# Optimization experiments

Measured on AMD Instinct MI355X. Metric: run time of the kernel, lower is better.

Reference implementation:

```python
import jax, jax.numpy as jnp
import numpy as np

B, T, D, DIM = 32, 2048, 1024, 1024


def setup_inputs() -> dict:
    key = jax.random.key(0)
    ks = jax.random.split(key, 7)
    def glorot(k, shape):
        lim = np.sqrt(6.0 / (shape[0] + shape[1]))
        return jax.random.uniform(k, shape, jnp.float32, -lim, lim)
    return {
        "input_states": jax.random.normal(ks[0], (B, T, D), jnp.float32),
        "last_state": jax.random.normal(ks[1], (B, D), jnp.float32),
        "Wy": glorot(ks[2], (D, DIM)),
        "Wh": glorot(ks[3], (D, DIM)),
        "w": glorot(ks[4], (DIM, 1)),
        "Wp": glorot(ks[5], (D, DIM)),
        "Wx": glorot(ks[6], (D, DIM)),
    }


def reference(input_states, last_state, Wy, Wh, w, Wp, Wx):
    # hs: (B,T,dim); last_state projection broadcast over T (the original
    # tiles last_state via a ones-matmul; a plain broadcast is the same math)
    hs = jnp.einsum("btd,de->bte", input_states, Wy)
    hproj = last_state @ Wh                      # (B,dim)
    m = jax.nn.relu(hs + hproj[:, None, :])      # (B,T,dim)
    scores = jnp.einsum("bte,eo->bt", m, w[:, :1])  # squeeze last dim
    alpha = jax.nn.softmax(scores, axis=-1)      # (B,T)
    r = jnp.einsum("bt,btd->bd", alpha, input_states)
    out = jax.nn.relu(r @ Wp + last_state @ Wx)  # (B,dim)
    return out
```

## Files before the change

### kernel.cpp

```cpp
#include <hip/hip_runtime.h>
#include <hip/hip_bf16.h>
#include <stdint.h>

#define BB 32
#define TT 2048
#define DD 1024
#define DIMQ 1024
#define MTOT (BB*TT)

typedef __attribute__((ext_vector_type(8))) __bf16 bf16x8;
typedef __attribute__((ext_vector_type(4))) float f32x4;

__device__ __forceinline__ unsigned short f2bf(float f) {
    unsigned int u = __float_as_uint(f);
    u += 0x7FFF + ((u >> 16) & 1);
    return (unsigned short)(u >> 16);
}
__device__ __forceinline__ float bf2f(unsigned short s) {
    return __uint_as_float(((unsigned int)s) << 16);
}

__device__ __forceinline__ void load_lds16(const void* g, void* l) {
    __builtin_amdgcn_global_load_lds(
        (const __attribute__((address_space(1))) unsigned int*)g,
        (__attribute__((address_space(3))) unsigned int*)l,
        16, 0, 0);
}

__global__ void cast_x(const float* __restrict__ x, unsigned short* __restrict__ xb) {
    long i = ((long)blockIdx.x * blockDim.x + threadIdx.x) * 4;
    float4 a = *(const float4*)(x + i);
    ushort4 o;
    o.x = f2bf(a.x); o.y = f2bf(a.y); o.z = f2bf(a.z); o.w = f2bf(a.w);
    *(ushort4*)(xb + i) = o;
}

__global__ void transpose_cast(const float* __restrict__ Wsrc, unsigned short* __restrict__ Wdst) {
    __shared__ float tile[32][33];
    int bx = blockIdx.x * 32;
    int by = blockIdx.y * 32;
    int tx = threadIdx.x & 31;
    int ty4 = (threadIdx.x >> 5) * 4;
    #pragma unroll
    for (int r = 0; r < 4; r++)
        tile[ty4 + r][tx] = Wsrc[(size_t)(by + ty4 + r) * DIMQ + bx + tx];
    __syncthreads();
    #pragma unroll
    for (int r = 0; r < 4; r++)
        Wdst[(size_t)(bx + ty4 + r) * DD + by + tx] = f2bf(tile[tx][ty4 + r]);
}

__global__ void vecmat2(const float* __restrict__ last,
                        const float* __restrict__ Wh, const float* __restrict__ Wx,
                        float* __restrict__ hproj, float* __restrict__ lsWx) {
    __shared__ float vs[DD];
    __shared__ float red[4][64];
    int b = blockIdx.y;
    int e0 = blockIdx.x * 64;
    const float* Mat = blockIdx.z ? Wx : Wh;
    float* outp = blockIdx.z ? lsWx : hproj;
    int tid = threadIdx.x;
    for (int d = tid; d < DD; d += 256) vs[d] = last[b * DD + d];
    __syncthreads();
    int e = tid & 63, dg = tid >> 6;
    int d0 = dg * 256;
    const float* Mp = Mat + (size_t)d0 * DIMQ + e0 + e;
    float acc = 0.f;
    #pragma unroll 8
    for (int d = 0; d < 256; d++) acc += vs[d0 + d] * Mp[(size_t)d * DIMQ];
    red[dg][e] = acc;
    __syncthreads();
    if (dg == 0)
        outp[b * DIMQ + e0 + e] = red[0][e] + red[1][e] + red[2][e] + red[3][e];
}

__global__ __launch_bounds__(512, 2)
void gemm_scores(const unsigned short* __restrict__ Xb,
                 const unsigned short* __restrict__ WyT,
                 const float* __restrict__ hproj,
                 const float* __restrict__ wvec,
                 float* __restrict__ partials) {
    __shared__ unsigned short lds[65536];
    __shared__ float lp[256];

    int tid = threadIdx.x;
    int lane = tid & 63;
    int wave = tid >> 6;
    int wr = wave >> 2;
    int wc = wave & 3;

    int bidx = blockIdx.x;
    int rr = bidx & 255, rnd = bidx >> 8;
    int xcd = rr & 7, slot = rr >> 3;
    int ntile = slot & 3;
    int mtile = rnd * 64 + xcd * 8 + (slot >> 2);

    if (tid < 256) lp[tid] = 0.f;

    int ssub = wave >> 1, sks = wave & 1;
    const unsigned short* aG = Xb  + (size_t)(mtile * 256 + ssub * 16 + (lane & 15)) * DD + sks * 32 + (lane >> 4) * 8;
    const unsigned short* bG = WyT + (size_t)(ntile * 256 + ssub * 16 + (lane & 15)) * DD + sks * 32 + (lane >> 4) * 8;
    unsigned short* ldsAst = &lds[(ssub * 128 + sks * 64 + lane) * 8];
    unsigned short* ldsBst = ldsAst + 16384;

    const unsigned short* aRd = &lds[wr * 8192 + lane * 8];
    const unsigned short* bRd = &lds[16384 + (wc >> 1) * 8192 + (wc & 1) * 4096 + lane * 8];

#define STAGE_A(B_, H_, T_) { \
    const unsigned short* g_ = aG + (size_t)(H_) * 131072 + (T_) * 64; \
    load_lds16(g_,         ldsAst + (B_) * 32768 + (H_) * 8192);       \
    load_lds16(g_ + 65536, ldsAst + (B_) * 32768 + (H_) * 8192 + 4096); }
#define STAGE_B(B_, H_, T_) { \
    const unsigned short* g_ = bG + (size_t)(H_) * 131072 + (T_) * 64; \
    load_lds16(g_,         ldsBst + (B_) * 32768 + (H_) * 8192);       \
    load_lds16(g_ + 65536, ldsBst + (B_) * 32768 + (H_) * 8192 + 4096); }

    f32x4 acc[8][4] = {};
    bf16x8 af[4][2], bfr[4][2];

#define LDA(B_, MH) { \
    _Pragma("unroll") for (int i_ = 0; i_ < 4; i_++) \
    _Pragma("unroll") for (int k_ = 0; k_ < 2; k_++) \
        af[i_][k_] = *reinterpret_cast<const bf16x8*>(aRd + (B_) * 32768 + ((MH) * 4 + i_) * 1024 + k_ * 512); }
#define LDB(B_, NH) { \
    _Pragma("unroll") for (int j_ = 0; j_ < 2; j_++) \
    _Pragma("unroll") for (int k_ = 0; k_ < 2; k_++) \
        bfr[(NH) * 2 + j_][k_] = *reinterpret_cast<const bf16x8*>(bRd + (B_) * 32768 + ((NH) * 2 + j_) * 1024 + k_ * 512); }
#define MFMA_Q(MH, NH) { \
    _Pragma("unroll") for (int k_ = 0; k_ < 2; k_++) \
    _Pragma("unroll") for (int i_ = 0; i_ < 4; i_++) \
    _Pragma("unroll") for (int j_ = 0; j_ < 2; j_++) \
        acc[(MH) * 4 + i_][(NH) * 2 + j_] = __builtin_amdgcn_mfma_f32_16x16x32_bf16( \
            af[i_][k_], bfr[(NH) * 2 + j_][k_], acc[(MH) * 4 + i_][(NH) * 2 + j_], 0, 0, 0); }

#define BAR() __builtin_amdgcn_s_barrier()
#define LGKM0() { asm volatile("s_waitcnt lgkmcnt(0)" ::: "memory"); __builtin_amdgcn_sched_barrier(0); }
#define VM4() asm volatile("s_waitcnt vmcnt(4)" ::: "memory")
#define PRIO1() __builtin_amdgcn_s_setprio(1)
#define PRIO0() __builtin_amdgcn_s_setprio(0)

    STAGE_B(0, 0, 0); STAGE_B(0, 1, 0);
    STAGE_A(0, 0, 0); STAGE_A(0, 1, 0);
    STAGE_B(1, 0, 1); STAGE_B(1, 1, 1);
    VM4();
    BAR();

    for (int it = 0; it < 8; ++it) {
        int t1  = 2 * it + 1;
        int tp0 = 2 * it + 2; if (tp0 > 14) tp0 = 14;
        int tp1 = 2 * it + 3; if (tp1 > 15) tp1 = 15;

        LDA(0, 0); LDB(0, 0); STAGE_A(1, 0, t1);
        BAR(); LGKM0(); PRIO1(); MFMA_Q(0, 0); PRIO0(); BAR();
        LDB(0, 1); STAGE_A(1, 1, t1);
        BAR(); LGKM0(); PRIO1(); MFMA_Q(0, 1); PRIO0(); BAR();
        LDA(0, 1); STAGE_B(0, 0, tp0);
        BAR(); LGKM0(); PRIO1(); MFMA_Q(1, 1); PRIO0(); BAR();
        STAGE_B(0, 1, tp0);
        BAR(); PRIO1(); MFMA_Q(1, 0); PRIO0(); VM4(); BAR();
        LDA(1, 0); LDB(1, 0); STAGE_A(0, 0, tp0);
        BAR(); LGKM0(); PRIO1(); MFMA_Q(0, 0); PRIO0(); BAR();
        LDB(1, 1); STAGE_A(0, 1, tp0);
        BAR(); LGKM0(); PRIO1(); MFMA_Q(0, 1); PRIO0(); BAR();
        LDA(1, 1); STAGE_B(1, 0, tp1);
        BAR(); LGKM0(); PRIO1(); MFMA_Q(1, 1); PRIO0(); BAR();
        STAGE_B(1, 1, tp1);
        BAR(); PRIO1(); MFMA_Q(1, 0); PRIO0(); VM4(); BAR();
    }

    __syncthreads();

    int bIdx = mtile >> 3;
    int q = lane >> 4, l15 = lane & 15;

    float hpv[4], wvv[4];
    #pragma unroll
    for (int nf = 0; nf < 4; nf++) {
        int n = ntile * 256 + wc * 64 + nf * 16 + l15;
        hpv[nf] = hproj[bIdx * DIMQ + n];
        wvv[nf] = wvec[n];
    }

    #pragma unroll
    for (int m = 0; m < 8; m++) {
        f32x4 s = {0.f, 0.f, 0.f, 0.f};
        #pragma unroll
        for (int nf = 0; nf < 4; nf++) {
            #pragma unroll
            for (int r = 0; r < 4; r++) {
                float v = acc[m][nf][r] + hpv[nf];
                v = v > 0.f ? v : 0.f;
                s[r] += v * wvv[nf];
            }
        }
        #pragma unroll
        for (int off = 1; off < 16; off <<= 1) {
            s[0] += __shfl_xor(s[0], off);
            s[1] += __shfl_xor(s[1], off);
            s[2] += __shfl_xor(s[2], off);
            s[3] += __shfl_xor(s[3], off);
        }
        if (l15 == 0) {
            int mrow = wr * 128 + m * 16 + q * 4;
            atomicAdd(&lp[mrow + 0], s[0]);
            atomicAdd(&lp[mrow + 1], s[1]);
            atomicAdd(&lp[mrow + 2], s[2]);
            atomicAdd(&lp[mrow + 3], s[3]);
        }
    }
    __syncthreads();
    if (tid < 256)
        partials[(size_t)ntile * MTOT + mtile * 256 + tid] = lp[tid];

#undef STAGE_A
#undef STAGE_B
#undef LDA
#undef LDB
#undef MFMA_Q
#undef BAR
#undef LGKM0
#undef VM4
#undef PRIO1
#undef PRIO0
}

__global__ void softmax_alpha(const float* __restrict__ partials, float* __restrict__ alpha) {
    __shared__ float wred[4];
    __shared__ float wsum[4];
    int b = blockIdx.x;
    int tid = threadIdx.x;
    float s[8];
    float mx = -1e30f;
    #pragma unroll
    for (int c = 0; c < 8; c++) {
        int t = b * TT + tid + c * 256;
        float v = 0.f;
        #pragma unroll
        for (int p = 0; p < 4; p++) v += partials[(size_t)p * MTOT + t];
        s[c] = v;
        mx = fmaxf(mx, v);
    }
    for (int off = 32; off; off >>= 1) mx = fmaxf(mx, __shfl_xor(mx, off));
    if ((tid & 63) == 0) wred[tid >> 6] = mx;
    __syncthreads();
    mx = fmaxf(fmaxf(wred[0], wred[1]), fmaxf(wred[2], wred[3]));
    float sum = 0.f;
    #pragma unroll
    for (int c = 0; c < 8; c++) { s[c] = expf(s[c] - mx); sum += s[c]; }
    for (int off = 32; off; off >>= 1) sum += __shfl_xor(sum, off);
    if ((tid & 63) == 0) wsum[tid >> 6] = sum;
    __syncthreads();
    sum = wsum[0] + wsum[1] + wsum[2] + wsum[3];
    float inv = 1.f / sum;
    #pragma unroll
    for (int c = 0; c < 8; c++) alpha[b * TT + tid + c * 256] = s[c] * inv;
}

__global__ void weighted_sum(const unsigned short* __restrict__ Xb,
                             const float* __restrict__ alpha,
                             float* __restrict__ r_part) {
    __shared__ float al[128];
    int tc = blockIdx.x, b = blockIdx.y, tid = threadIdx.x;
    if (tid < 128) al[tid] = alpha[b * TT + tc * 128 + tid];
    __syncthreads();
    int d0 = tid * 4;
    const unsigned short* base = Xb + ((size_t)(b * TT + tc * 128)) * DD + d0;
    f32x4 acc = {0.f, 0.f, 0.f, 0.f};
    #pragma unroll 2
    for (int t = 0; t < 128; t++) {
        ushort4 xv = *(const ushort4*)(base + (size_t)t * DD);
        float a_ = al[t];
        acc[0] += a_ * bf2f(xv.x);
        acc[1] += a_ * bf2f(xv.y);
        acc[2] += a_ * bf2f(xv.z);
        acc[3] += a_ * bf2f(xv.w);
    }
    float* o = r_part + ((size_t)tc * BB + b) * DD + d0;
    *(float4*)o = *(float4*)&acc;
}

__global__ void final_out(const float* __restrict__ r_part, const float* __restrict__ Wp,
                          const float* __restrict__ lsWx, float* __restrict__ out) {
    __shared__ float rs[DD];
    __shared__ float red[4][64];
    int b = blockIdx.y;
    int e0 = blockIdx.x * 64;
    int tid = threadIdx.x;
    for (int d = tid; d < DD; d += 256) {
        float v = 0.f;
        #pragma unroll
        for (int p = 0; p < 16; p++) v += r_part[((size_t)p * BB + b) * DD + d];
        rs[d] = v;
    }
    __syncthreads();
    int e = tid & 63, dg = tid >> 6;
    int d0 = dg * 256;
    const float* Mp = Wp + (size_t)d0 * DIMQ + e0 + e;
    float acc = 0.f;
    #pragma unroll 8
    for (int d = 0; d < 256; d++) acc += rs[d0 + d] * Mp[(size_t)d * DIMQ];
    red[dg][e] = acc;
    __syncthreads();
    if (dg == 0) {
        float v = red[0][e] + red[1][e] + red[2][e] + red[3][e]
                + lsWx[b * DIMQ + e0 + e];
        out[b * DIMQ + e0 + e] = fmaxf(v, 0.f);
    }
}

extern "C" void kernel_launch(void* const* d_in, const int* in_sizes, int n_in,
                              void* d_out, int out_size, void* d_ws, size_t ws_size,
                              hipStream_t stream) {
    const float* x    = (const float*)d_in[0];
    const float* last = (const float*)d_in[1];
    const float* Wy   = (const float*)d_in[2];
    const float* Wh   = (const float*)d_in[3];
    const float* w    = (const float*)d_in[4];
    const float* Wp   = (const float*)d_in[5];
    const float* Wx   = (const float*)d_in[6];
    float* out = (float*)d_out;

    char* ws = (char*)d_ws;
    unsigned short* Xb   = (unsigned short*)(ws);
    unsigned short* WyT  = (unsigned short*)(ws + 134217728);
    float* hproj         = (float*)(ws + 136314880);
    float* lsWx          = (float*)(ws + 136445952);
    float* partials      = (float*)(ws + 136577024);
    float* alpha         = (float*)(ws + 137625600);
    float* r_part        = (float*)(ws + 137887744);

    cast_x<<<BB*TT*DD/4/256, 256, 0, stream>>>(x, Xb);
    transpose_cast<<<dim3(32, 32), 256, 0, stream>>>(Wy, WyT);
    vecmat2<<<dim3(DIMQ/64, BB, 2), 256, 0, stream>>>(last, Wh, Wx, hproj, lsWx);
    gemm_scores<<<1024, 512, 0, stream>>>(Xb, WyT, hproj, w, partials);
    softmax_alpha<<<BB, 256, 0, stream>>>(partials, alpha);
    weighted_sum<<<dim3(TT/128, BB), 256, 0, stream>>>(Xb, alpha, r_part);
    final_out<<<dim3(DIMQ/64, BB), 256, 0, stream>>>(r_part, Wp, lsWx, out);
}
```

Measured before the change: 626.1 us.

## Restructure GEMM main loop into simpler double-buffered per-tile pipeline

Replaces the 8-phase ping-pong schedule, which had many barriers and interleaved partial stages, with a per-K-tile loop. Each iteration waits for one whole tile (vmcnt 8), runs the MFMAs for both M halves and issues the stage of the full tile two steps ahead into the freed buffer. This cuts the barrier count per tile and drops the sched_barrier, letting the compiler schedule more freely. The cost is coarser overlap: a whole tile is prefetched at once rather than quarter by quarter, and with lgkm waits placed differently some LDS latency may be exposed.

```diff
diff --git a/kernel.cpp b/kernel.cpp
--- a/kernel.cpp
+++ b/kernel.cpp
@@ -106,26 +106,28 @@
     const unsigned short* aRd = &lds[wr * 8192 + lane * 8];
     const unsigned short* bRd = &lds[16384 + (wc >> 1) * 8192 + (wc & 1) * 4096 + lane * 8];
 
-#define STAGE_A(B_, H_, T_) { \
+#define STAGE_A(S_, H_, T_) { \
     const unsigned short* g_ = aG + (size_t)(H_) * 131072 + (T_) * 64; \
-    load_lds16(g_,         ldsAst + (B_) * 32768 + (H_) * 8192);       \
-    load_lds16(g_ + 65536, ldsAst + (B_) * 32768 + (H_) * 8192 + 4096); }
-#define STAGE_B(B_, H_, T_) { \
+    load_lds16(g_,         ldsAst + (S_) * 32768 + (H_) * 8192);       \
+    load_lds16(g_ + 65536, ldsAst + (S_) * 32768 + (H_) * 8192 + 4096); }
+#define STAGE_B(S_, H_, T_) { \
     const unsigned short* g_ = bG + (size_t)(H_) * 131072 + (T_) * 64; \
-    load_lds16(g_,         ldsBst + (B_) * 32768 + (H_) * 8192);       \
-    load_lds16(g_ + 65536, ldsBst + (B_) * 32768 + (H_) * 8192 + 4096); }
+    load_lds16(g_,         ldsBst + (S_) * 32768 + (H_) * 8192);       \
+    load_lds16(g_ + 65536, ldsBst + (S_) * 32768 + (H_) * 8192 + 4096); }
+#define STAGE_TILE(S_, T_) { STAGE_A(S_, 0, T_); STAGE_A(S_, 1, T_); \
+                             STAGE_B(S_, 0, T_); STAGE_B(S_, 1, T_); }
 
     f32x4 acc[8][4] = {};
     bf16x8 af[4][2], bfr[4][2];
 
-#define LDA(B_, MH) { \
+#define LDA(S_, MH) { \
     _Pragma("unroll") for (int i_ = 0; i_ < 4; i_++) \
     _Pragma("unroll") for (int k_ = 0; k_ < 2; k_++) \
-        af[i_][k_] = *reinterpret_cast<const bf16x8*>(aRd + (B_) * 32768 + ((MH) * 4 + i_) * 1024 + k_ * 512); }
-#define LDB(B_, NH) { \
+        af[i_][k_] = *reinterpret_cast<const bf16x8*>(aRd + (S_) * 32768 + ((MH) * 4 + i_) * 1024 + k_ * 512); }
+#define LDB(S_, NH) { \
     _Pragma("unroll") for (int j_ = 0; j_ < 2; j_++) \
     _Pragma("unroll") for (int k_ = 0; k_ < 2; k_++) \
-        bfr[(NH) * 2 + j_][k_] = *reinterpret_cast<const bf16x8*>(bRd + (B_) * 32768 + ((NH) * 2 + j_) * 1024 + k_ * 512); }
+        bfr[(NH) * 2 + j_][k_] = *reinterpret_cast<const bf16x8*>(bRd + (S_) * 32768 + ((NH) * 2 + j_) * 1024 + k_ * 512); }
 #define MFMA_Q(MH, NH) { \
     _Pragma("unroll") for (int k_ = 0; k_ < 2; k_++) \
     _Pragma("unroll") for (int i_ = 0; i_ < 4; i_++) \
@@ -134,38 +136,32 @@
             af[i_][k_], bfr[(NH) * 2 + j_][k_], acc[(MH) * 4 + i_][(NH) * 2 + j_], 0, 0, 0); }
 
 #define BAR() __builtin_amdgcn_s_barrier()
-#define LGKM0() { asm volatile("s_waitcnt lgkmcnt(0)" ::: "memory"); __builtin_amdgcn_sched_barrier(0); }
-#define VM4() asm volatile("s_waitcnt vmcnt(4)" ::: "memory")
+#define LGKM0() asm volatile("s_waitcnt lgkmcnt(0)" ::: "memory")
+#define VMW8() asm volatile("s_waitcnt vmcnt(8)" ::: "memory")
 #define PRIO1() __builtin_amdgcn_s_setprio(1)
 #define PRIO0() __builtin_amdgcn_s_setprio(0)
 
-    STAGE_B(0, 0, 0); STAGE_B(0, 1, 0);
-    STAGE_A(0, 0, 0); STAGE_A(0, 1, 0);
-    STAGE_B(1, 0, 1); STAGE_B(1, 1, 1);
-    VM4();
-    BAR();
-
-    for (int it = 0; it < 8; ++it) {
-        int t1  = 2 * it + 1;
-        int tp0 = 2 * it + 2; if (tp0 > 14) tp0 = 14;
-        int tp1 = 2 * it + 3; if (tp1 > 15) tp1 = 15;
-
-        LDA(0, 0); LDB(0, 0); STAGE_A(1, 0, t1);
-        BAR(); LGKM0(); PRIO1(); MFMA_Q(0, 0); PRIO0(); BAR();
-        LDB(0, 1); STAGE_A(1, 1, t1);
-        BAR(); LGKM0(); PRIO1(); MFMA_Q(0, 1); PRIO0(); BAR();
-        LDA(0, 1); STAGE_B(0, 0, tp0);
-        BAR(); LGKM0(); PRIO1(); MFMA_Q(1, 1); PRIO0(); BAR();
-        STAGE_B(0, 1, tp0);
-        BAR(); PRIO1(); MFMA_Q(1, 0); PRIO0(); VM4(); BAR();
-        LDA(1, 0); LDB(1, 0); STAGE_A(0, 0, tp0);
-        BAR(); LGKM0(); PRIO1(); MFMA_Q(0, 0); PRIO0(); BAR();
-        LDB(1, 1); STAGE_A(0, 1, tp0);
-        BAR(); LGKM0(); PRIO1(); MFMA_Q(0, 1); PRIO0(); BAR();
-        LDA(1, 1); STAGE_B(1, 0, tp1);
-        BAR(); LGKM0(); PRIO1(); MFMA_Q(1, 1); PRIO0(); BAR();
-        STAGE_B(1, 1, tp1);
-        BAR(); PRIO1(); MFMA_Q(1, 0); PRIO0(); VM4(); BAR();
+    STAGE_TILE(0, 0);
+    STAGE_TILE(1, 1);
+
+    #pragma unroll 2
+    for (int t = 0; t < 16; ++t) {
+        int s = t & 1;
+        int tp = (t + 2 > 15) ? 15 : (t + 2);
+
+        VMW8();
+        BAR();
+
+        LDB(s, 0); LDB(s, 1);
+        LDA(s, 0);
+        PRIO1(); MFMA_Q(0, 0); MFMA_Q(0, 1); PRIO0();
+
+        LDA(s, 1);
+        LGKM0();
+        BAR();
+
+        STAGE_TILE(s, tp);
+        PRIO1(); MFMA_Q(1, 0); MFMA_Q(1, 1); PRIO0();
     }
 
     __syncthreads();
@@ -214,12 +210,13 @@
 
 #undef STAGE_A
 #undef STAGE_B
+#undef STAGE_TILE
 #undef LDA
 #undef LDB
 #undef MFMA_Q
 #undef BAR
 #undef LGKM0
-#undef VM4
+#undef VMW8
 #undef PRIO1
 #undef PRIO0
 }
```

After: 621.8 us. About the same (-0.7%).
